# Kernel optimization log

Measured on AMD Instinct MI355X. Metric: run time of the kernel, lower is better.

Reference implementation:

```python
import jax, jax.numpy as jnp
import numpy as np

H = 2048  # hidden_dim


def setup_inputs() -> dict:
    key = jax.random.key(0)
    ks = jax.random.split(key, 7)
    s = 1.0 / np.sqrt(H)
    x = jax.random.normal(ks[0], (4, 2048, H), dtype=jnp.float32)
    Wq = jax.random.uniform(ks[1], (H, H), jnp.float32, -s, s)
    Wk = jax.random.uniform(ks[2], (H, H), jnp.float32, -s, s)
    Wv = jax.random.uniform(ks[3], (H, H), jnp.float32, -s, s)
    Wo = jax.random.uniform(ks[4], (H, H), jnp.float32, -s, s)
    W1 = jax.random.uniform(ks[5], (H, H), jnp.float32, -s, s)
    W2 = jax.random.uniform(ks[6], (H, H), jnp.float32, -s, s)
    return {"x": x, "Wq": Wq, "Wk": Wk, "Wv": Wv, "Wo": Wo, "W1": W1, "W2": W2}


def reference(x, Wq, Wk, Wv, Wo, W1, W2):
    # Attention (single head, no 1/sqrt(d) scaling, no mask "" faithful to source)
    q = jnp.einsum('bsh,dh->bsd', x, Wq)
    k = jnp.einsum('bsh,dh->bsd', x, Wk)
    v = jnp.einsum('bsh,dh->bsd', x, Wv)
    score = jax.nn.softmax(jnp.einsum('bqd,bkd->bqk', q, k), axis=-1)
    attn = jnp.einsum('bqk,bkd->bqd', score, v)
    attn = jnp.einsum('bsh,dh->bsd', attn, Wo)
    # FFN
    h = jax.nn.relu(jnp.einsum('bsh,dh->bsd', attn, W1))
    y = jnp.einsum('bsh,dh->bsd', h, W2)
    return jnp.sum(y)
```

## Files before the change

kernel.cpp:

```cpp
#include <hip/hip_runtime.h>
#include <hip/hip_bf16.h>
#include <stdint.h>

typedef _Float16 h16_t;
typedef __attribute__((ext_vector_type(8))) _Float16 h16x8;
typedef __attribute__((ext_vector_type(4))) _Float16 h16x4;
typedef __attribute__((ext_vector_type(16))) float f32x16;

static constexpr int HDIM  = 2048;
static constexpr int MROWS = 8192;

__device__ __forceinline__ void gload_lds16(const h16_t* g, h16_t* l) {
  __builtin_amdgcn_global_load_lds(
      (const __attribute__((address_space(1))) void*)g,
      (__attribute__((address_space(3))) void*)l, 16, 0, 0);
}

__device__ __forceinline__ uint32_t ldsaddr(const void* p) {
  return (uint32_t)(uintptr_t)(const __attribute__((address_space(3))) void*)p;
}

__device__ __forceinline__ h16x8 dsread(uint32_t off) {
  h16x8 r;
  asm volatile("ds_read_b128 %0, %1" : "=v"(r) : "v"(off));
  return r;
}

__device__ __forceinline__ void bar()    { __builtin_amdgcn_s_barrier(); }
__device__ __forceinline__ void waitlg0(){ asm volatile("s_waitcnt lgkmcnt(0)" ::: "memory");
                                           __builtin_amdgcn_sched_barrier(0); }
__device__ __forceinline__ void waitlg4(){ asm volatile("s_waitcnt lgkmcnt(4)" ::: "memory");
                                           __builtin_amdgcn_sched_barrier(0); }
__device__ __forceinline__ void waitlg8(){ asm volatile("s_waitcnt lgkmcnt(8)" ::: "memory");
                                           __builtin_amdgcn_sched_barrier(0); }
__device__ __forceinline__ void waitvm4(){ asm volatile("s_waitcnt vmcnt(4)" ::: "memory"); }
__device__ __forceinline__ void waitvm0(){ asm volatile("s_waitcnt vmcnt(0)" ::: "memory"); }

__device__ __forceinline__ void gemm_core(const h16_t* __restrict__ A,
                                          const h16_t* __restrict__ B,
                                          f32x16 acc[2][2],
                                          h16_t* sA, h16_t* sB) {
  const int tid  = threadIdx.x;
  const int wid  = tid >> 6;
  const int lane = tid & 63;
  const int wr  = (wid >> 1) << 6;
  const int wc  = (wid & 1) << 6;
  const int l31 = lane & 31;
  const int hi  = lane >> 5;
  const int sx  = lane & 7;

#pragma unroll
  for (int i = 0; i < 2; i++)
#pragma unroll
    for (int j = 0; j < 2; j++)
#pragma unroll
      for (int r = 0; r < 16; r++) acc[i][j][r] = 0.0f;

  for (int k0 = 0; k0 < 2048; k0 += 64) {
    __syncthreads();
#pragma unroll
    for (int rnd = 0; rnd < 4; rnd++) {
      const int cid  = rnd * 256 + tid;
      const int row  = cid >> 3;
      const int koct = (cid & 7) ^ (row & 7);
      const long long goff = (long long)row * 2048 + k0 + koct * 8;
      gload_lds16(A + goff, sA + (rnd * 256 + wid * 64) * 8);
      gload_lds16(B + goff, sB + (rnd * 256 + wid * 64) * 8);
    }
    __syncthreads();

#pragma unroll
    for (int ko = 0; ko < 4; ko++) {
      const int po = (2 * ko + hi) ^ sx;
      h16x8 fa[2], fb[2];
#pragma unroll
      for (int i = 0; i < 2; i++)
        fa[i] = *(const h16x8*)(sA + (wr + i * 32 + l31) * 64 + po * 8);
#pragma unroll
      for (int j = 0; j < 2; j++)
        fb[j] = *(const h16x8*)(sB + (wc + j * 32 + l31) * 64 + po * 8);
#pragma unroll
      for (int i = 0; i < 2; i++)
#pragma unroll
        for (int j = 0; j < 2; j++)
          acc[i][j] = __builtin_amdgcn_mfma_f32_32x32x16_f16(
              fa[i], fb[j], acc[i][j], 0, 0, 0);
    }
  }
}

__device__ __forceinline__ void store_c(h16_t* __restrict__ C,
                                        f32x16 acc[2][2], int bm, int bn) {
  const int tid  = threadIdx.x;
  const int wid  = tid >> 6;
  const int lane = tid & 63;
  const int wr = (wid >> 1) << 6, wc = (wid & 1) << 6;
  const int l31 = lane & 31, hi = lane >> 5;
  const int gr = bm * 128 + wr + 4 * hi;
  const int gc = bn * 128 + wc + l31;
#pragma unroll
  for (int i = 0; i < 2; i++)
#pragma unroll
    for (int r = 0; r < 16; r++) {
      const int row = gr + i * 32 + (r & 3) + 8 * (r >> 2);
      const long long ro = (long long)row * 2048;
#pragma unroll
      for (int j = 0; j < 2; j++)
        C[ro + gc + j * 32] = (h16_t)acc[i][j][r];
    }
}

__global__ __launch_bounds__(256)
void gemm_b(const h16_t* __restrict__ Ab, const h16_t* __restrict__ Bb,
            h16_t* __restrict__ Cb, long long sAz, long long sBz, long long sCz)
{
  __shared__ __align__(16) h16_t sA[128 * 64];
  __shared__ __align__(16) h16_t sB[128 * 64];
  const int bn = blockIdx.x, bm = blockIdx.y, z = blockIdx.z;
  const h16_t* A = Ab + (long long)z * sAz + (long long)bm * 128 * 2048;
  const h16_t* B = Bb + (long long)z * sBz + (long long)bn * 128 * 2048;
  f32x16 acc[2][2];
  gemm_core(A, B, acc, sA, sB);
  store_c(Cb + (long long)z * sCz, acc, bm, bn);
}

__device__ __forceinline__ void core256(const h16_t* __restrict__ A,
                                        const h16_t* __restrict__ B,
                                        h16_t* smem, f32x16 acc[4][2])
{
  const int tid  = threadIdx.x;
  const int wid  = tid >> 6, lane = tid & 63;
  const int wr2  = wid >> 2, wcid = wid & 3;
  const int l31  = lane & 31, hi = lane >> 5, sx = lane & 7;

  h16_t* pA[2] = { smem,          smem + 32768 };
  h16_t* pB[2] = { smem + 16384,  smem + 49152 };

  uint32_t poB[4];
#pragma unroll
  for (int ks = 0; ks < 4; ks++) poB[ks] = (uint32_t)((((2 * ks + hi) ^ sx) << 4));
  const uint32_t lrow = (uint32_t)(l31 * 128);
  const uint32_t aT0 = ldsaddr(pA[0]) + (uint32_t)(wr2 * 16384) + lrow;
  const uint32_t aT1 = ldsaddr(pA[1]) + (uint32_t)(wr2 * 16384) + lrow;
  const uint32_t bT0 = ldsaddr(pB[0]) + (uint32_t)(wcid * 8192) + lrow;
  const uint32_t bT1 = ldsaddr(pB[1]) + (uint32_t)(wcid * 8192) + lrow;

  const int srow = tid >> 3;
  const long long stOff = (long long)srow * HDIM + (long long)(((tid & 7) ^ (srow & 7)) * 8);
  const int dOff = tid * 8;

  auto stage1 = [&](const h16_t* M, h16_t* panel, int k0, int ci) {
    gload_lds16(M + stOff + k0 + (long long)ci * (64 * HDIM),
                panel + ci * 4096 + dOff);
  };

#pragma unroll
  for (int i = 0; i < 4; i++)
#pragma unroll
    for (int j = 0; j < 2; j++)
#pragma unroll
      for (int r = 0; r < 16; r++) acc[i][j][r] = 0.0f;

  h16x8 fA[2][4], fB0[4], fB1[4];

  auto rdA = [&](uint32_t base) {
#pragma unroll
    for (int mi = 0; mi < 2; mi++)
#pragma unroll
      for (int ks = 0; ks < 4; ks++)
        fA[mi][ks] = dsread(base + (uint32_t)(mi * 4096) + poB[ks]);
  };
  auto rdB = [&](h16x8 (&fb)[4], uint32_t base) {
#pragma unroll
    for (int ks = 0; ks < 4; ks++) fb[ks] = dsread(base + poB[ks]);
  };
  auto mm8 = [&](int am0, int nj, h16x8 (&fb)[4]) {
#pragma unroll
    for (int ks = 0; ks < 4; ks++)
#pragma unroll
      for (int mi = 0; mi < 2; mi++)
        acc[am0 + mi][nj] = __builtin_amdgcn_mfma_f32_32x32x16_f16(
            fA[mi][ks], fb[ks], acc[am0 + mi][nj], 0, 0, 0);
  };

  auto tileX = [&](uint32_t aT, uint32_t bT, h16_t* pAcur,
                   h16_t* stB, int kB, bool doB,
                   int kA, bool doA, int tailmode) {
    rdA(aT);
    rdB(fB0, bT);
    rdB(fB1, bT + 4096);
    if (doB) { stage1(B, stB, kB, 0); stage1(B, stB, kB, 1);
               stage1(B, stB, kB, 2); stage1(B, stB, kB, 3); }
    waitlg8();
    bar();
    if (doA) { stage1(A, pAcur, kA, 0); stage1(A, pAcur, kA, 2); }
    waitlg4();
    __builtin_amdgcn_s_setprio(1); mm8(0, 0, fB0); __builtin_amdgcn_s_setprio(0);
    waitlg0();
    __builtin_amdgcn_s_setprio(1); mm8(0, 1, fB1); __builtin_amdgcn_s_setprio(0);
    rdA(aT + 8192);
    waitlg0();
    bar();
    if (doA) { stage1(A, pAcur, kA, 1); stage1(A, pAcur, kA, 3); }
    __builtin_amdgcn_s_setprio(1); mm8(2, 1, fB1); __builtin_amdgcn_s_setprio(0);
    __builtin_amdgcn_s_setprio(1); mm8(2, 0, fB0); __builtin_amdgcn_s_setprio(0);
    if (tailmode == 0) waitvm4(); else if (tailmode == 1) waitvm0();
    bar();
  };

  stage1(A, pA[0], 0, 0); stage1(A, pA[0], 0, 1);
  stage1(A, pA[0], 0, 2); stage1(A, pA[0], 0, 3);
  stage1(B, pB[0], 0, 0); stage1(B, pB[0], 0, 1);
  stage1(B, pB[0], 0, 2); stage1(B, pB[0], 0, 3);
  stage1(A, pA[1], 64, 0); stage1(A, pA[1], 64, 1);
  stage1(A, pA[1], 64, 2); stage1(A, pA[1], 64, 3);
  waitvm4(); bar();

#pragma unroll 1
  for (int t = 0; t < 30; t += 2) {
    tileX(aT0, bT0, pA[0], pB[1], (t + 1) * 64, true, (t + 2) * 64, true, 0);
    tileX(aT1, bT1, pA[1], pB[0], (t + 2) * 64, true, (t + 3) * 64, true, 0);
  }
  tileX(aT0, bT0, pA[0], pB[1], 31 * 64, true, 0, false, 1);
  tileX(aT1, bT1, pA[1], nullptr, 0, false, 0, false, 2);
}

__device__ __forceinline__ void store256(h16_t* __restrict__ C,
                                         f32x16 acc[4][2], int bm, int bn)
{
  const int tid = threadIdx.x, wid = tid >> 6, lane = tid & 63;
  const int wr2 = wid >> 2, wcid = wid & 3;
  const int l31 = lane & 31, hi = lane >> 5;
  const int gr0 = bm * 256 + wr2 * 128 + 4 * hi;
  const int gc0 = bn * 256 + wcid * 64 + l31;
#pragma unroll
  for (int am = 0; am < 4; am++)
#pragma unroll
    for (int r = 0; r < 16; r++) {
      const int row = gr0 + am * 32 + (r & 3) + 8 * (r >> 2);
      const long long ro = (long long)row * HDIM;
#pragma unroll
      for (int nj = 0; nj < 2; nj++)
        C[ro + gc0 + nj * 32] = (h16_t)acc[am][nj][r];
    }
}

template<int GY>
__device__ __forceinline__ void remap256(int& bn, int& bm, int& z) {
  const int flat = blockIdx.x + 8 * (blockIdx.y + GY * blockIdx.z);
  const int l = (flat & 7) * 32 + (flat >> 3);
  bn = l & 7;
  const int rest = l >> 3;
  bm = rest & (GY - 1);
  z  = rest / GY;
}

template<int GY>
__global__ __launch_bounds__(512, 1)
void gemm256_b(const h16_t* __restrict__ Ab, const h16_t* __restrict__ Bb,
               h16_t* __restrict__ Cb, long long sAz, long long sBz, long long sCz)
{
  __shared__ __align__(16) h16_t smem[4 * 16384];
  int bn, bm, z;
  remap256<GY>(bn, bm, z);
  const h16_t* A = Ab + (long long)z * sAz + (long long)bm * 256 * HDIM;
  const h16_t* B = Bb + (long long)z * sBz + (long long)bn * 256 * HDIM;
  f32x16 acc[4][2];
  core256(A, B, smem, acc);
  store256(Cb + (long long)z * sCz, acc, bm, bn);
}

__global__ __launch_bounds__(512)
void softmax_kernel(h16_t* __restrict__ sc)
{
  const int tid = threadIdx.x, wid = tid >> 6, lane = tid & 63;
  const long long row = (long long)blockIdx.x * 8 + wid;
  h16_t* s = sc + row * HDIM;
  h16x8 raw[4];
#pragma unroll
  for (int i = 0; i < 4; i++) raw[i] = ((const h16x8*)s)[i * 64 + lane];
  float v[32];
  float mx = -3.0e38f;
#pragma unroll
  for (int i = 0; i < 32; i++) { v[i] = (float)raw[i >> 3][i & 7]; mx = fmaxf(mx, v[i]); }
#pragma unroll
  for (int off = 32; off; off >>= 1) mx = fmaxf(mx, __shfl_xor(mx, off, 64));
  float sum = 0.f;
#pragma unroll
  for (int i = 0; i < 32; i++) { v[i] = __expf(v[i] - mx); sum += v[i]; }
#pragma unroll
  for (int off = 32; off; off >>= 1) sum += __shfl_xor(sum, off, 64);
  const float inv = 1.0f / sum;
#pragma unroll
  for (int i = 0; i < 4; i++) {
    h16x8 o;
#pragma unroll
    for (int j = 0; j < 8; j++) o[j] = (h16_t)(v[i * 8 + j] * inv);
    ((h16x8*)s)[i * 64 + lane] = o;
  }
}

__global__ __launch_bounds__(512, 1)
void gemm256_final(const h16_t* __restrict__ P, const h16_t* __restrict__ utb,
                   const float* __restrict__ w2p, float* __restrict__ outp)
{
  __shared__ __align__(16) h16_t smem[4 * 16384];
  int bn, bm, z;
  remap256<8>(bn, bm, z);
  const long long HH = (long long)HDIM * HDIM;
  const h16_t* A = P   + (long long)z * HH + (long long)bm * 256 * HDIM;
  const h16_t* B = utb + (long long)z * HH + (long long)bn * 256 * HDIM;
  f32x16 acc[4][2];
  core256(A, B, smem, acc);

  const int tid = threadIdx.x, wid = tid >> 6, lane = tid & 63;
  const int wcid = wid & 3, l31 = lane & 31;
  const int gc0 = bn * 256 + wcid * 64 + l31;
  float w2j[2];
#pragma unroll
  for (int nj = 0; nj < 2; nj++) {
    const int col = gc0 + nj * 32;
    float s = 0.f;
#pragma unroll
    for (int c = 0; c < 32; c++) s += w2p[c * HDIM + col];
    w2j[nj] = s;
  }
  float s = 0.f;
#pragma unroll
  for (int am = 0; am < 4; am++)
#pragma unroll
    for (int nj = 0; nj < 2; nj++)
#pragma unroll
      for (int r = 0; r < 16; r++) {
        const float vv = acc[am][nj][r];
        s += (vv > 0.f) ? vv * w2j[nj] : 0.f;
      }
#pragma unroll
  for (int off = 32; off; off >>= 1) s += __shfl_down(s, off, 64);
  __shared__ float red[8];
  if (lane == 0) red[wid] = s;
  __syncthreads();
  if (tid == 0) {
    float t = 0.f;
#pragma unroll
    for (int w = 0; w < 8; w++) t += red[w];
    atomicAdd(outp, t);
  }
}

__global__ __launch_bounds__(256)
void prologue_kernel(const float* __restrict__ x,  const float* __restrict__ Wq,
                     const float* __restrict__ Wk, const float* __restrict__ Wv,
                     const float* __restrict__ Wo, const float* __restrict__ W1,
                     const float* __restrict__ W2,
                     h16_t* __restrict__ xb,  h16_t* __restrict__ WkT,
                     h16_t* __restrict__ WvT, h16_t* __restrict__ WqT,
                     h16_t* __restrict__ Wob, h16_t* __restrict__ W1b,
                     float* __restrict__ w2p, float* __restrict__ outp)
{
  const int t = threadIdx.x;
  int b = blockIdx.x;
  if (b < 16384) {
    const long long i = (long long)b * 256 + t;
    const float4 v = ((const float4*)x)[i];
    h16x4 o;
    o[0] = (h16_t)v.x; o[1] = (h16_t)v.y; o[2] = (h16_t)v.z; o[3] = (h16_t)v.w;
    ((h16x4*)xb)[i] = o;
    return;
  }
  b -= 16384;
  if (b < 3072) {
    const float* src; h16_t* dst;
    const int w = b >> 10, b10 = b & 1023;
    if (w == 0)      { src = Wk; dst = WkT; }
    else if (w == 1) { src = Wv; dst = WvT; }
    else             { src = Wq; dst = WqT; }
    __shared__ float tl[64][65];
    const int bx = (b10 & 31) * 64, by = (b10 >> 5) * 64;
#pragma unroll
    for (int i = 0; i < 4; i++) {
      const int idx = i * 256 + t;
      const int r = idx >> 4, c4 = idx & 15;
      const float4 v = *(const float4*)(src + (long long)(by + r) * 2048 + bx + c4 * 4);
      tl[r][c4 * 4 + 0] = v.x; tl[r][c4 * 4 + 1] = v.y;
      tl[r][c4 * 4 + 2] = v.z; tl[r][c4 * 4 + 3] = v.w;
    }
    __syncthreads();
#pragma unroll
    for (int i = 0; i < 2; i++) {
      const int idx = i * 256 + t;
      const int c = idx >> 3, r8 = (idx & 7) * 8;
      h16x8 o;
#pragma unroll
      for (int j = 0; j < 8; j++) o[j] = (h16_t)tl[r8 + j][c];
      *(h16x8*)(dst + (long long)(bx + c) * 2048 + by + r8) = o;
    }
    return;
  }
  b -= 3072;
  if (b < 8192) {
    const float* src = (b < 4096) ? Wo : W1;
    h16_t* dst = (b < 4096) ? Wob : W1b;
    const long long i = (long long)(b & 4095) * 256 + t;
    const float4 v = ((const float4*)src)[i];
    h16x4 o;
    o[0] = (h16_t)v.x; o[1] = (h16_t)v.y; o[2] = (h16_t)v.z; o[3] = (h16_t)v.w;
    ((h16x4*)dst)[i] = o;
    return;
  }
  b -= 8192;
  if (b < 256) {
    const int c = b >> 3;
    const int h = (b & 7) * 256 + t;
    float s = 0.f;
#pragma unroll 4
    for (int d = 0; d < 64; d++) s += W2[(long long)(c * 64 + d) * 2048 + h];
    w2p[c * 2048 + h] = s;
    return;
  }
  b -= 256;
  if (b == 0 && t == 0) outp[0] = 0.f;
}

extern "C" void kernel_launch(void* const* d_in, const int* in_sizes, int n_in,
                              void* d_out, int out_size, void* d_ws, size_t ws_size,
                              hipStream_t stream)
{
  const float* x  = (const float*)d_in[0];
  const float* Wq = (const float*)d_in[1];
  const float* Wk = (const float*)d_in[2];
  const float* Wv = (const float*)d_in[3];
  const float* Wo = (const float*)d_in[4];
  const float* W1 = (const float*)d_in[5];
  const float* W2 = (const float*)d_in[6];
  float* out = (float*)d_out;

  const long long HH = (long long)HDIM * HDIM;
  const long long XE = (long long)MROWS * HDIM;

  char* p = (char*)d_ws;
  h16_t* xb   = (h16_t*)p; p += XE * 2;
  h16_t* WkT  = (h16_t*)p; p += HH * 2;
  h16_t* WvT  = (h16_t*)p; p += HH * 2;
  h16_t* WqT  = (h16_t*)p; p += HH * 2;
  h16_t* Wob  = (h16_t*)p; p += HH * 2;
  h16_t* WqkT = (h16_t*)p; p += HH * 2;
  h16_t* GT   = (h16_t*)p; p += HH * 2;
  h16_t* W1b  = (h16_t*)p; p += HH * 2;
  h16_t* Wvow = (h16_t*)p; p += HH * 2;
  h16_t* tb   = (h16_t*)p; p += XE * 2;
  h16_t* sc   = (h16_t*)p; p += XE * 2;
  float* w2p  = (float*)p; p += 32 * HDIM * 4;

  const dim3 b256(256), b512(512);

  prologue_kernel<<<dim3(16384 + 3072 + 8192 + 256 + 1), b256, 0, stream>>>(
      x, Wq, Wk, Wv, Wo, W1, W2, xb, WkT, WvT, WqT, Wob, W1b, w2p, out);

  gemm_b<<<dim3(16, 16, 2), b256, 0, stream>>>(WkT, WqT, WqkT, HH, HH, HH);

  gemm_b<<<dim3(16, 16, 1), b256, 0, stream>>>(W1b, GT, Wvow, 0, 0, 0);

  gemm256_b<32><<<dim3(8, 32, 1), b512, 0, stream>>>(xb, WqkT, tb, 0, 0, 0);

  gemm256_b<8><<<dim3(8, 8, 4), b512, 0, stream>>>(tb, xb, sc, HH, HH, HH);

  softmax_kernel<<<dim3(1024), b512, 0, stream>>>(sc);

  gemm256_b<8><<<dim3(8, 8, 4), b512, 0, stream>>>(Wvow, xb, tb, 0, HH, HH);

  gemm256_final<<<dim3(8, 8, 4), b512, 0, stream>>>(sc, tb, w2p, out);
}
```

Before: 533.9 us.

## Add 128x256 tile GEMM kernel with higher occupancy for two projection GEMMs

```diff
diff --git a/kernel.cpp b/kernel.cpp
--- a/kernel.cpp
+++ b/kernel.cpp
@@ -34,6 +34,7 @@
 __device__ __forceinline__ void waitlg8(){ asm volatile("s_waitcnt lgkmcnt(8)" ::: "memory");
                                            __builtin_amdgcn_sched_barrier(0); }
 __device__ __forceinline__ void waitvm4(){ asm volatile("s_waitcnt vmcnt(4)" ::: "memory"); }
+__device__ __forceinline__ void waitvm1(){ asm volatile("s_waitcnt vmcnt(1)" ::: "memory"); }
 __device__ __forceinline__ void waitvm0(){ asm volatile("s_waitcnt vmcnt(0)" ::: "memory"); }
 
 __device__ __forceinline__ void gemm_core(const h16_t* __restrict__ A,
@@ -270,6 +271,135 @@
   store256(Cb + (long long)z * sCz, acc, bm, bn);
 }
 
+__device__ __forceinline__ void core2b(const h16_t* __restrict__ A,
+                                       const h16_t* __restrict__ B,
+                                       h16_t* smem, f32x16 acc[2][2])
+{
+  const int tid  = threadIdx.x;
+  const int wid  = tid >> 6, lane = tid & 63;
+  const int wr2  = wid >> 2, wcid = wid & 3;
+  const int l31  = lane & 31, hi = lane >> 5, s3 = lane & 3;
+
+  h16_t* pA[2] = { smem,          smem + 12288 };
+  h16_t* pB[2] = { smem + 4096,   smem + 16384 };
+
+  uint32_t po[2];
+#pragma unroll
+  for (int ks = 0; ks < 2; ks++) po[ks] = (uint32_t)((((2 * ks + hi) ^ s3) << 4));
+  const uint32_t lrow = (uint32_t)(l31 * 64);
+  const uint32_t aT0 = ldsaddr(pA[0]) + (uint32_t)(wr2 * 4096) + lrow;
+  const uint32_t aT1 = ldsaddr(pA[1]) + (uint32_t)(wr2 * 4096) + lrow;
+  const uint32_t bT0 = ldsaddr(pB[0]) + (uint32_t)(wcid * 4096) + lrow;
+  const uint32_t bT1 = ldsaddr(pB[1]) + (uint32_t)(wcid * 4096) + lrow;
+
+  const int srow = tid >> 2;
+  const long long stOff = (long long)srow * HDIM + (long long)(((tid & 3) ^ (srow & 3)) * 8);
+  const int dOff = tid * 8;
+
+  auto stageA = [&](h16_t* panel, int k0) {
+    gload_lds16(A + stOff + k0, panel + dOff);
+  };
+  auto stageB = [&](h16_t* panel, int k0, int ci) {
+    gload_lds16(B + stOff + k0 + (long long)ci * (128 * HDIM),
+                panel + ci * 4096 + dOff);
+  };
+
+#pragma unroll
+  for (int i = 0; i < 2; i++)
+#pragma unroll
+    for (int j = 0; j < 2; j++)
+#pragma unroll
+      for (int r = 0; r < 16; r++) acc[i][j][r] = 0.0f;
+
+  h16x8 fA[2][2], fB[2][2];
+
+  auto tileY = [&](uint32_t aT, uint32_t bT, h16_t* pAcur,
+                   h16_t* stB, int kB, bool doB,
+                   int kA, bool doA, int tailmode) {
+#pragma unroll
+    for (int mi = 0; mi < 2; mi++)
+#pragma unroll
+      for (int ks = 0; ks < 2; ks++)
+        fA[mi][ks] = dsread(aT + (uint32_t)(mi * 2048) + po[ks]);
+#pragma unroll
+    for (int nj = 0; nj < 2; nj++)
+#pragma unroll
+      for (int ks = 0; ks < 2; ks++)
+        fB[nj][ks] = dsread(bT + (uint32_t)(nj * 2048) + po[ks]);
+    if (doB) { stageB(stB, kB, 0); stageB(stB, kB, 1); }
+    waitlg4();
+    bar();
+    if (doA) stageA(pAcur, kA);
+    waitlg0();
+    __builtin_amdgcn_s_setprio(1);
+#pragma unroll
+    for (int ks = 0; ks < 2; ks++)
+#pragma unroll
+      for (int mi = 0; mi < 2; mi++)
+#pragma unroll
+        for (int nj = 0; nj < 2; nj++)
+          acc[mi][nj] = __builtin_amdgcn_mfma_f32_32x32x16_f16(
+              fA[mi][ks], fB[nj][ks], acc[mi][nj], 0, 0, 0);
+    __builtin_amdgcn_s_setprio(0);
+    if (tailmode == 0) waitvm1(); else if (tailmode == 1) waitvm0();
+    bar();
+  };
+
+  stageA(pA[0], 0);
+  stageB(pB[0], 0, 0); stageB(pB[0], 0, 1);
+  stageA(pA[1], 32);
+  waitvm1(); bar();
+
+#pragma unroll 1
+  for (int tp = 0; tp < 31; tp++) {
+    const int t = 2 * tp;
+    tileY(aT0, bT0, pA[0], pB[1], (t + 1) * 32, true, (t + 2) * 32, true, 0);
+    tileY(aT1, bT1, pA[1], pB[0], (t + 2) * 32, true, (t + 3) * 32, true, 0);
+  }
+  tileY(aT0, bT0, pA[0], pB[1], 63 * 32, true, 0, false, 1);
+  tileY(aT1, bT1, pA[1], nullptr, 0, false, 0, false, 2);
+}
+
+__device__ __forceinline__ void store2b(h16_t* __restrict__ C,
+                                        f32x16 acc[2][2], int bm, int bn)
+{
+  const int tid = threadIdx.x, wid = tid >> 6, lane = tid & 63;
+  const int wr2 = wid >> 2, wcid = wid & 3;
+  const int l31 = lane & 31, hi = lane >> 5;
+  const int gr0 = bm * 128 + wr2 * 64 + 4 * hi;
+  const int gc0 = bn * 256 + wcid * 64 + l31;
+#pragma unroll
+  for (int am = 0; am < 2; am++)
+#pragma unroll
+    for (int r = 0; r < 16; r++) {
+      const int row = gr0 + am * 32 + (r & 3) + 8 * (r >> 2);
+      const long long ro = (long long)row * HDIM;
+#pragma unroll
+      for (int nj = 0; nj < 2; nj++)
+        C[ro + gc0 + nj * 32] = (h16_t)acc[am][nj][r];
+    }
+}
+
+template<int GY>
+__global__ __launch_bounds__(512, 4)
+void gemm2b(const h16_t* __restrict__ Ab, const h16_t* __restrict__ Bb,
+            h16_t* __restrict__ Cb, long long sAz, long long sBz, long long sCz)
+{
+  __shared__ __align__(16) h16_t smem[24576];
+  const int flat = blockIdx.x + 8 * (blockIdx.y + GY * blockIdx.z);
+  const int CH = GY * (int)gridDim.z;
+  const int l = (flat & 7) * CH + (flat >> 3);
+  const int bn = l & 7;
+  const int rest = l >> 3;
+  const int bm = rest & (GY - 1);
+  const int z  = rest / GY;
+  const h16_t* A = Ab + (long long)z * sAz + (long long)bm * 128 * HDIM;
+  const h16_t* B = Bb + (long long)z * sBz + (long long)bn * 256 * HDIM;
+  f32x16 acc[2][2];
+  core2b(A, B, smem, acc);
+  store2b(Cb + (long long)z * sCz, acc, bm, bn);
+}
+
 __global__ __launch_bounds__(512)
 void softmax_kernel(h16_t* __restrict__ sc)
 {
@@ -461,13 +591,13 @@
 
   gemm_b<<<dim3(16, 16, 1), b256, 0, stream>>>(W1b, GT, Wvow, 0, 0, 0);
 
-  gemm256_b<32><<<dim3(8, 32, 1), b512, 0, stream>>>(xb, WqkT, tb, 0, 0, 0);
+  gemm2b<64><<<dim3(8, 64, 1), b512, 0, stream>>>(xb, WqkT, tb, 0, 0, 0);
 
   gemm256_b<8><<<dim3(8, 8, 4), b512, 0, stream>>>(tb, xb, sc, HH, HH, HH);
 
   softmax_kernel<<<dim3(1024), b512, 0, stream>>>(sc);
 
-  gemm256_b<8><<<dim3(8, 8, 4), b512, 0, stream>>>(Wvow, xb, tb, 0, HH, HH);
+  gemm2b<16><<<dim3(8, 16, 4), b512, 0, stream>>>(Wvow, xb, tb, 0, HH, HH);
 
   gemm256_final<<<dim3(8, 8, 4), b512, 0, stream>>>(sc, tb, w2p, out);
 }
```

New measurement: 582.0 us. 1.09x slower.
